# Kernel optimization log

Hardware: AMD Instinct MI355X
Metric: run time of the kernel (lower is better)

Reference implementation:

```python
import jax, jax.numpy as jnp
import numpy as np

POOL = 7  # adaptive_avg_pool2d output size (7,7)


def _bin_edges(start, length):
    """Adaptive-avg-pool bin boundaries.
    start, length: [N] int32 -> (lo, hi) each [N, POOL] absolute indices,
    matching torch: lo_i = floor(i*L/P), hi_i = ceil((i+1)*L/P).
    """
    i = jnp.arange(POOL, dtype=jnp.int32)
    lo = start[:, None] + (i[None, :] * length[:, None]) // POOL
    hi = start[:, None] + (-((-(i[None, :] + 1)) * length[:, None] // POOL))
    # note: ceil(a/b) = -(-a // b); written below explicitly
    hi = start[:, None] - ((-(i[None, :] + 1) * length[:, None]) // POOL)
    return lo, hi


def roi_adaptive_avg_pool(features, rois):
    """features: [1, C, H, W]; rois: [N, 4] int (x1,y1,x2,y2 inclusive).
    Returns [N, C, POOL, POOL] == torch stack of adaptive_avg_pool2d over
    features[:, :, y1:y2+1, x1:x2+1], vectorized via an integral image.
    """
    B, C, H, W = features.shape  # B == 1 (forced by shared_fcs input dim)
    # integral image with a zero row/col prepended: ii[y, x] = sum over [:y, :x]
    ii = jnp.cumsum(jnp.cumsum(features, axis=2), axis=3)
    ii = jnp.pad(ii, ((0, 0), (0, 0), (1, 0), (1, 0)))[0]  # [C, H+1, W+1]

    x1, y1, x2, y2 = rois[:, 0], rois[:, 1], rois[:, 2], rois[:, 3]
    ys, ye = _bin_edges(y1, y2 - y1 + 1)   # [N, POOL]
    xs, xe = _bin_edges(x1, x2 - x1 + 1)
    Y0, Y1 = ys[:, :, None], ye[:, :, None]   # [N, POOL, 1]
    X0, X1 = xs[:, None, :], xe[:, None, :]   # [N, 1, POOL]

    def gather(Y, X):
        return ii[:, Y, X]  # [C, N, POOL, POOL]

    sums = gather(Y1, X1) - gather(Y0, X1) - gather(Y1, X0) + gather(Y0, X0)
    area = ((Y1 - Y0) * (X1 - X0)).astype(features.dtype)  # [N, POOL, POOL]
    pooled = sums / area[None]                              # [C, N, POOL, POOL]
    return jnp.transpose(pooled, (1, 0, 2, 3))              # [N, C, POOL, POOL]


def setup_inputs() -> dict:
    key = jax.random.key(0)
    ks = jax.random.split(key, 12)
    C, H, W, N, F = 256, 336, 336, 2000, 256
    features = jax.random.normal(ks[0], (1, C, H, W), dtype=jnp.float32)
    # valid small ROIs (shuttlecock-sized), x1<=x2, y1<=y2, in-bounds
    x1 = jax.random.randint(ks[1], (N,), 0, W - 40)
    y1 = jax.random.randint(ks[2], (N,), 0, H - 40)
    bw = jax.random.randint(ks[3], (N,), 4, 40)
    bh = jax.random.randint(ks[4], (N,), 4, 40)
    rois = jnp.stack([x1, y1, jnp.minimum(x1 + bw, W - 1),
                      jnp.minimum(y1 + bh, H - 1)], axis=1).astype(jnp.int32)
    d_in = C * POOL * POOL
    w1 = jax.random.normal(ks[5], (d_in, F), dtype=jnp.float32) * (1.0 / np.sqrt(d_in))
    b1 = jnp.zeros((F,), dtype=jnp.float32)
    w2 = jax.random.normal(ks[6], (F, F), dtype=jnp.float32) * (1.0 / np.sqrt(F))
    b2 = jnp.zeros((F,), dtype=jnp.float32)
    w_cls = jax.random.normal(ks[7], (F, 2), dtype=jnp.float32) * 0.01
    b_cls = jnp.zeros((2,), dtype=jnp.float32)
    w_reg = jax.random.normal(ks[8], (F, 4), dtype=jnp.float32) * 0.001
    b_reg = jnp.zeros((4,), dtype=jnp.float32)
    return {"features": features, "rois": rois, "w1": w1, "b1": b1,
            "w2": w2, "b2": b2, "w_cls": w_cls, "b_cls": b_cls,
            "w_reg": w_reg, "b_reg": b_reg}


def reference(features, rois, w1, b1, w2, b2, w_cls, b_cls, w_reg, b_reg):
    roi_feats = roi_adaptive_avg_pool(features, rois)          # [N, C, 7, 7]
    roi_feats = roi_feats.reshape(roi_feats.shape[0], -1)      # [N, C*49]
    h = jax.nn.relu(roi_feats @ w1 + b1)
    h = jax.nn.relu(h @ w2 + b2)
    cls_score = h @ w_cls + b_cls                              # [N, num_classes+1]
    bbox_pred = h @ w_reg + b_reg                              # [N, 4]
    return (cls_score, bbox_pred)
```

## Files before the change

### kernel.cpp

```cpp
#include <hip/hip_runtime.h>

typedef unsigned int uint;
typedef unsigned short ushort;
typedef __bf16 v8bf __attribute__((ext_vector_type(8)));
typedef float v4f __attribute__((ext_vector_type(4)));

#define CCH 256
#define HH 336
#define WW 336
#define HWSZ (HH*WW)
#define NROI 2000
#define KDIM 12544
#define MPAD 2048
#define SPLITK 14
#define KSP (KDIM/SPLITK)

__device__ __forceinline__ ushort bf16r(float f) {
  uint u = __float_as_uint(f);
  u += 0x7fffu + ((u >> 16) & 1u);
  return (ushort)(u >> 16);
}
__device__ __forceinline__ uint packbf(float a, float b) {
  return (uint)bf16r(a) | ((uint)bf16r(b) << 16);
}

typedef const __attribute__((address_space(1))) uint* gas_t;
typedef __attribute__((address_space(3))) uint* las_t;
__device__ __forceinline__ void async16(const void* g, void* l) {
  __builtin_amdgcn_global_load_lds((gas_t)g, (las_t)l, 16, 0, 0);
}

__global__ __launch_bounds__(256) void k_transpose(const float* __restrict__ f,
                                                   uint* __restrict__ ftu) {
  __shared__ uint T[64 * 132];
  int tid = threadIdx.x;
  int hw0 = blockIdx.x * 64;
  int hwl = tid & 63;
  int cq = tid >> 6;
  int hw = hw0 + hwl;
#pragma unroll 4
  for (int it = 0; it < 32; ++it) {
    int c = it * 8 + cq * 2;
    float a = f[(size_t)c * HWSZ + hw];
    float b = f[(size_t)(c + 1) * HWSZ + hw];
    T[hwl * 132 + it * 4 + cq] = packbf(a, b);
  }
  __syncthreads();
  int co = tid & 31, r = tid >> 5;
#pragma unroll
  for (int i = 0; i < 8; ++i) {
    int hwr = i * 8 + r;
    uint4 v = *(const uint4*)&T[hwr * 132 + co * 4];
    *(uint4*)(ftu + (size_t)(hw0 + hwr) * 128 + co * 4) = v;
  }
}

__global__ __launch_bounds__(256) void k_w1perm(const float* __restrict__ w1,
                                                uint* __restrict__ w1t_u) {
  int bin = blockIdx.x % 49;
  int c0 = (blockIdx.x / 49) * 32;
  __shared__ ushort T[32][258];
  int n = threadIdx.x;
  for (int i = 0; i < 32; ++i)
    T[i][n] = bf16r(w1[(size_t)((c0 + i) * 49 + bin) * 256 + n]);
  __syncthreads();
  int cc = threadIdx.x & 15;
  int nb = threadIdx.x >> 4;
  for (int rep = 0; rep < 16; ++rep) {
    int nn = rep * 16 + nb;
    uint v = (uint)T[2 * cc][nn] | ((uint)T[2 * cc + 1][nn] << 16);
    w1t_u[(size_t)nn * (KDIM / 2) + bin * 128 + c0 / 2 + cc] = v;
  }
}

__global__ __launch_bounds__(256) void k_w2t(const float* __restrict__ w2,
                                             ushort* __restrict__ w2t) {
  int n = blockIdx.x, k = threadIdx.x;
  w2t[n * 256 + k] = bf16r(w2[k * 256 + n]);
}

__global__ __launch_bounds__(256) void k_sort(const int* __restrict__ rois,
                                              int* __restrict__ perm) {
  __shared__ int hist[64];
  __shared__ int keys[NROI];
  int tid = threadIdx.x;
  if (tid < 64) hist[tid] = 0;
  __syncthreads();
  for (int i = tid; i < NROI; i += 256) {
    int x1 = rois[i * 4 + 0], y1 = rois[i * 4 + 1];
    int x2 = rois[i * 4 + 2], y2 = rois[i * 4 + 3];
    int cx = (x1 + x2) >> 1, cy = (y1 + y2) >> 1;
    int k = (cy / 42) * 8 + (cx / 42);
    keys[i] = k;
    atomicAdd(&hist[k], 1);
  }
  __syncthreads();
  if (tid == 0) {
    int s = 0;
    for (int b = 0; b < 64; ++b) { int c = hist[b]; hist[b] = s; s += c; }
  }
  __syncthreads();
  for (int i = tid; i < NROI; i += 256) {
    int pos = atomicAdd(&hist[keys[i]], 1);
    perm[pos] = i;
  }
}

#define UNPK8(A, u) do {                                     \
  A[0] += __uint_as_float((u).x << 16);                      \
  A[1] += __uint_as_float((u).x & 0xffff0000u);              \
  A[2] += __uint_as_float((u).y << 16);                      \
  A[3] += __uint_as_float((u).y & 0xffff0000u);              \
  A[4] += __uint_as_float((u).z << 16);                      \
  A[5] += __uint_as_float((u).z & 0xffff0000u);              \
  A[6] += __uint_as_float((u).w << 16);                      \
  A[7] += __uint_as_float((u).w & 0xffff0000u);              \
} while (0)

__global__ __launch_bounds__(64) void k_pool(const int* __restrict__ rois,
                                             const int* __restrict__ perm,
                                             const uint4* __restrict__ ft4,
                                             uint4* __restrict__ rf4) {
  int bx = blockIdx.x;
  int slot = (bx & 7) * 250 + (bx >> 3);
  int n = perm[slot];
  int wv = blockIdx.y;
  int t = threadIdx.x;
  int co = t & 31, par = t >> 5;
  int x1 = rois[n * 4 + 0], y1 = rois[n * 4 + 1];
  int x2 = rois[n * 4 + 2], y2 = rois[n * 4 + 3];
  int Lw = x2 - x1 + 1, Lh = y2 - y1 + 1;
  int ylo = y1 + (wv * Lh) / 7;
  int yhi = y1 + ((wv + 1) * Lh + 6) / 7;
  int rh = yhi - ylo;
  uint ob = (uint)n * 1568 + (uint)wv * 224 + co;
  for (int b = 0; b < 7; ++b) {
    int lo = x1 + (b * Lw) / 7;
    int hi = x1 + ((b + 1) * Lw + 6) / 7;
    float a[8], c[8];
#pragma unroll
    for (int j = 0; j < 8; ++j) { a[j] = 0.f; c[j] = 0.f; }
    for (int y = ylo; y < yhi; ++y) {
      const uint4* p = ft4 + (size_t)(y * WW + lo + par) * 32 + co;
      int x = lo + par;
      for (; x + 2 < hi; x += 4) {
        uint4 u0 = p[0], u1 = p[64];
        p += 128;
        UNPK8(a, u0);
        UNPK8(c, u1);
      }
      for (; x < hi; x += 2) {
        uint4 u = p[0];
        p += 64;
        UNPK8(a, u);
      }
    }
#pragma unroll
    for (int j = 0; j < 8; ++j) a[j] += c[j];
#pragma unroll
    for (int j = 0; j < 8; ++j) a[j] += __shfl_xor(a[j], 32, 64);
    if (t < 32) {
      float inv = 1.0f / (float)(rh * (hi - lo));
      uint4 o;
      o.x = packbf(a[0] * inv, a[1] * inv);
      o.y = packbf(a[2] * inv, a[3] * inv);
      o.z = packbf(a[4] * inv, a[5] * inv);
      o.w = packbf(a[6] * inv, a[7] * inv);
      rf4[ob + b * 32] = o;
    }
  }
}

__global__ __launch_bounds__(256) void k_gemm1(const ushort* __restrict__ A,
                                               const ushort* __restrict__ B,
                                               float* __restrict__ P) {
  __shared__ ushort As[128 * 64];
  __shared__ ushort Bs[128 * 64];
  int m0 = blockIdx.x * 128;
  int n0 = blockIdx.y * 128;
  int ks = blockIdx.z;
  int k0 = ks * KSP;
  int tid = threadIdx.x;
  int lane = tid & 63, wv = tid >> 6;
  int wm = wv >> 1, wn = wv & 1;
  int lm = lane & 15, quad = lane >> 4;
  int srow = tid >> 3, scol = (tid & 7) * 8;
  v4f acc[4][4];
#pragma unroll
  for (int i = 0; i < 4; ++i)
#pragma unroll
    for (int j = 0; j < 4; ++j) acc[i][j] = (v4f){0.f, 0.f, 0.f, 0.f};
  const ushort* Ab = A + (size_t)(m0 + srow) * KDIM + k0 + scol;
  const ushort* Bb = B + (size_t)(n0 + srow) * KDIM + k0 + scol;
  for (int kt = 0; kt < KSP / 64; ++kt) {
    __syncthreads();
#pragma unroll
    for (int r = 0; r < 4; ++r)
      async16(Ab + (size_t)(r * 32) * KDIM + kt * 64, &As[(srow + r * 32) * 64 + scol]);
#pragma unroll
    for (int r = 0; r < 4; ++r)
      async16(Bb + (size_t)(r * 32) * KDIM + kt * 64, &Bs[(srow + r * 32) * 64 + scol]);
    __syncthreads();
#pragma unroll
    for (int kk = 0; kk < 64; kk += 32) {
      v8bf a[4], b[4];
#pragma unroll
      for (int i = 0; i < 4; ++i)
        a[i] = *(const v8bf*)&As[(wm * 64 + i * 16 + lm) * 64 + kk + quad * 8];
#pragma unroll
      for (int j = 0; j < 4; ++j)
        b[j] = *(const v8bf*)&Bs[(wn * 64 + j * 16 + lm) * 64 + kk + quad * 8];
#pragma unroll
      for (int i = 0; i < 4; ++i)
#pragma unroll
        for (int j = 0; j < 4; ++j)
          acc[i][j] = __builtin_amdgcn_mfma_f32_16x16x32_bf16(a[i], b[j], acc[i][j], 0, 0, 0);
    }
  }
  float* Pb = P + (size_t)ks * MPAD * 256;
#pragma unroll
  for (int i = 0; i < 4; ++i)
#pragma unroll
    for (int j = 0; j < 4; ++j) {
      int row = m0 + wm * 64 + i * 16 + quad * 4;
      int col = n0 + wn * 64 + j * 16 + lm;
#pragma unroll
      for (int r = 0; r < 4; ++r)
        Pb[(size_t)(row + r) * 256 + col] = acc[i][j][r];
    }
}

__global__ __launch_bounds__(256) void k_reduce(const float* __restrict__ P,
                                                const float* __restrict__ b1,
                                                uint* __restrict__ h1u) {
  int idx = blockIdx.x * 256 + threadIdx.x;
  int m = idx >> 7, np = idx & 127;
  const float2* Pp = (const float2*)P;
  float2 s = {0.f, 0.f};
#pragma unroll
  for (int ks = 0; ks < SPLITK; ++ks) {
    float2 v = Pp[(size_t)(ks * MPAD + m) * 128 + np];
    s.x += v.x; s.y += v.y;
  }
  s.x += b1[2 * np]; s.y += b1[2 * np + 1];
  s.x = fmaxf(s.x, 0.f); s.y = fmaxf(s.y, 0.f);
  h1u[idx] = packbf(s.x, s.y);
}

__global__ __launch_bounds__(256) void k_gemm2(const ushort* __restrict__ h1b,
                                               const ushort* __restrict__ w2t,
                                               const float* __restrict__ b2,
                                               const float* __restrict__ wcls,
                                               const float* __restrict__ bcls,
                                               const float* __restrict__ wreg,
                                               const float* __restrict__ breg,
                                               float* __restrict__ out) {
  __shared__ ushort As2[64 * 64];
  __shared__ ushort Bs2[256 * 64];
  __shared__ float Hs[64 * 257];
  int tid = threadIdx.x;
  int r0 = blockIdx.x * 64;
  int lane = tid & 63, wv = tid >> 6;
  int lm = lane & 15, quad = lane >> 4;
  int srow = tid >> 3, scol = (tid & 7) * 8;
  v4f acc[16];
#pragma unroll
  for (int j = 0; j < 16; ++j) acc[j] = (v4f){0.f, 0.f, 0.f, 0.f};
  for (int kt = 0; kt < 4; ++kt) {
    __syncthreads();
#pragma unroll
    for (int r = 0; r < 2; ++r)
      async16(h1b + (size_t)(r0 + srow + r * 32) * 256 + kt * 64 + scol,
              &As2[(srow + r * 32) * 64 + scol]);
#pragma unroll
    for (int r = 0; r < 8; ++r)
      async16(w2t + (size_t)(srow + r * 32) * 256 + kt * 64 + scol,
              &Bs2[(srow + r * 32) * 64 + scol]);
    __syncthreads();
#pragma unroll
    for (int kk = 0; kk < 64; kk += 32) {
      v8bf a = *(const v8bf*)&As2[(wv * 16 + lm) * 64 + kk + quad * 8];
#pragma unroll
      for (int j = 0; j < 16; ++j) {
        v8bf b = *(const v8bf*)&Bs2[(j * 16 + lm) * 64 + kk + quad * 8];
        acc[j] = __builtin_amdgcn_mfma_f32_16x16x32_bf16(a, b, acc[j], 0, 0, 0);
      }
    }
  }
#pragma unroll
  for (int j = 0; j < 16; ++j) {
    int nn = j * 16 + lm;
    float bb = b2[nn];
#pragma unroll
    for (int r = 0; r < 4; ++r) {
      int row = wv * 16 + quad * 4 + r;
      Hs[row * 257 + nn] = fmaxf(acc[j][r] + bb, 0.f);
    }
  }
  __syncthreads();
  for (int o = tid; o < 384; o += 256) {
    int hd = o >> 6, r = o & 63;
    int grow = r0 + r;
    float d = 0.f;
    if (hd < 2) {
      for (int k = 0; k < 256; ++k) d += Hs[r * 257 + k] * wcls[k * 2 + hd];
      d += bcls[hd];
      if (grow < NROI) out[grow * 2 + hd] = d;
    } else {
      int h4 = hd - 2;
      for (int k = 0; k < 256; ++k) d += Hs[r * 257 + k] * wreg[k * 4 + h4];
      d += breg[h4];
      if (grow < NROI) out[4000 + grow * 4 + h4] = d;
    }
  }
}

extern "C" void kernel_launch(void* const* d_in, const int* in_sizes, int n_in,
                              void* d_out, int out_size, void* d_ws, size_t ws_size,
                              hipStream_t stream) {
  const float* features = (const float*)d_in[0];
  const int* rois = (const int*)d_in[1];
  const float* w1 = (const float*)d_in[2];
  const float* b1 = (const float*)d_in[3];
  const float* w2 = (const float*)d_in[4];
  const float* b2 = (const float*)d_in[5];
  const float* wcls = (const float*)d_in[6];
  const float* bcls = (const float*)d_in[7];
  const float* wreg = (const float*)d_in[8];
  const float* breg = (const float*)d_in[9];
  char* ws = (char*)d_ws;
  ushort* ft  = (ushort*)(ws + 0);
  ushort* w1t = (ushort*)(ws + 57802752);
  ushort* w2t = (ushort*)(ws + 64225280);
  ushort* rf  = (ushort*)(ws + 64356352);
  int*    perm = (int*)(ws + 64356352 + (size_t)NROI * KDIM * 2);
  float*  P   = (float*)(ws + 115736576);
  ushort* h1b = (ushort*)(ws + 145096704);
  float* out = (float*)d_out;

  hipLaunchKernelGGL(k_transpose, dim3(HWSZ / 64), dim3(256), 0, stream,
                     features, (uint*)ft);
  hipLaunchKernelGGL(k_w1perm, dim3(392), dim3(256), 0, stream, w1, (uint*)w1t);
  hipLaunchKernelGGL(k_w2t, dim3(256), dim3(256), 0, stream, w2, w2t);
  hipLaunchKernelGGL(k_sort, dim3(1), dim3(256), 0, stream, rois, perm);
  hipLaunchKernelGGL(k_pool, dim3(NROI, 7), dim3(64), 0, stream, rois, perm,
                     (const uint4*)ft, (uint4*)rf);
  hipLaunchKernelGGL(k_gemm1, dim3(16, 2, SPLITK), dim3(256), 0, stream, rf, w1t, P);
  hipLaunchKernelGGL(k_reduce, dim3(1024), dim3(256), 0, stream, P, b1, (uint*)h1b);
  hipLaunchKernelGGL(k_gemm2, dim3(32), dim3(256), 0, stream, h1b, w2t, b2, wcls, bcls, wreg, breg, out);
}
```

Baseline: 354.0 us.

## Pad transpose LDS, parallel-scan sort histogram, flatten pool grid, shrink gemm1 M tile

Pads the transpose shared-memory row stride to 134 to cut bank conflicts, reading with two uint2 loads. The histogram prefix sum in the sort kernel becomes a wave-level shuffle scan instead of a serial loop on one thread. The pool kernel uses a 1D grid so the seven row-bins of one ROI get adjacent block indices, which should improve cache locality. gemm1 moves from 128x128 to 64x128 tiles, doubling block count for occupancy at the cost of more B-tile reloads.

```diff
diff --git a/kernel.cpp b/kernel.cpp
--- a/kernel.cpp
+++ b/kernel.cpp
@@ -32,7 +32,7 @@
 
 __global__ __launch_bounds__(256) void k_transpose(const float* __restrict__ f,
                                                    uint* __restrict__ ftu) {
-  __shared__ uint T[64 * 132];
+  __shared__ uint T[64 * 134];
   int tid = threadIdx.x;
   int hw0 = blockIdx.x * 64;
   int hwl = tid & 63;
@@ -43,15 +43,17 @@
     int c = it * 8 + cq * 2;
     float a = f[(size_t)c * HWSZ + hw];
     float b = f[(size_t)(c + 1) * HWSZ + hw];
-    T[hwl * 132 + it * 4 + cq] = packbf(a, b);
+    T[hwl * 134 + it * 4 + cq] = packbf(a, b);
   }
   __syncthreads();
   int co = tid & 31, r = tid >> 5;
 #pragma unroll
   for (int i = 0; i < 8; ++i) {
     int hwr = i * 8 + r;
-    uint4 v = *(const uint4*)&T[hwr * 132 + co * 4];
-    *(uint4*)(ftu + (size_t)(hw0 + hwr) * 128 + co * 4) = v;
+    uint2 v0 = *(const uint2*)&T[hwr * 134 + co * 4];
+    uint2 v1 = *(const uint2*)&T[hwr * 134 + co * 4 + 2];
+    *(uint4*)(ftu + (size_t)(hw0 + hwr) * 128 + co * 4) =
+        make_uint4(v0.x, v0.y, v1.x, v1.y);
   }
 }
 
@@ -95,9 +97,15 @@
     atomicAdd(&hist[k], 1);
   }
   __syncthreads();
-  if (tid == 0) {
-    int s = 0;
-    for (int b = 0; b < 64; ++b) { int c = hist[b]; hist[b] = s; s += c; }
+  if (tid < 64) {
+    int v = hist[tid];
+    int s = v;
+#pragma unroll
+    for (int d = 1; d < 64; d <<= 1) {
+      int t = __shfl_up(s, d, 64);
+      if (tid >= d) s += t;
+    }
+    hist[tid] = s - v;
   }
   __syncthreads();
   for (int i = tid; i < NROI; i += 256) {
@@ -121,19 +129,20 @@
                                              const int* __restrict__ perm,
                                              const uint4* __restrict__ ft4,
                                              uint4* __restrict__ rf4) {
-  int bx = blockIdx.x;
-  int slot = (bx & 7) * 250 + (bx >> 3);
+  int L = blockIdx.x;
+  int i = L >> 3;
+  int slot = (L & 7) * 250 + i / 7;
+  int by = i % 7;
   int n = perm[slot];
-  int wv = blockIdx.y;
   int t = threadIdx.x;
   int co = t & 31, par = t >> 5;
   int x1 = rois[n * 4 + 0], y1 = rois[n * 4 + 1];
   int x2 = rois[n * 4 + 2], y2 = rois[n * 4 + 3];
   int Lw = x2 - x1 + 1, Lh = y2 - y1 + 1;
-  int ylo = y1 + (wv * Lh) / 7;
-  int yhi = y1 + ((wv + 1) * Lh + 6) / 7;
+  int ylo = y1 + (by * Lh) / 7;
+  int yhi = y1 + ((by + 1) * Lh + 6) / 7;
   int rh = yhi - ylo;
-  uint ob = (uint)n * 1568 + (uint)wv * 224 + co;
+  uint ob = (uint)n * 1568 + (uint)by * 224 + co;
   for (int b = 0; b < 7; ++b) {
     int lo = x1 + (b * Lw) / 7;
     int hi = x1 + ((b + 1) * Lw + 6) / 7;
@@ -174,20 +183,20 @@
 __global__ __launch_bounds__(256) void k_gemm1(const ushort* __restrict__ A,
                                                const ushort* __restrict__ B,
                                                float* __restrict__ P) {
-  __shared__ ushort As[128 * 64];
+  __shared__ ushort As[64 * 64];
   __shared__ ushort Bs[128 * 64];
-  int m0 = blockIdx.x * 128;
+  int m0 = blockIdx.x * 64;
   int n0 = blockIdx.y * 128;
   int ks = blockIdx.z;
   int k0 = ks * KSP;
   int tid = threadIdx.x;
   int lane = tid & 63, wv = tid >> 6;
-  int wm = wv >> 1, wn = wv & 1;
+  int wm = wv & 1, wn = wv >> 1;
   int lm = lane & 15, quad = lane >> 4;
   int srow = tid >> 3, scol = (tid & 7) * 8;
-  v4f acc[4][4];
-#pragma unroll
-  for (int i = 0; i < 4; ++i)
+  v4f acc[2][4];
+#pragma unroll
+  for (int i = 0; i < 2; ++i)
 #pragma unroll
     for (int j = 0; j < 4; ++j) acc[i][j] = (v4f){0.f, 0.f, 0.f, 0.f};
   const ushort* Ab = A + (size_t)(m0 + srow) * KDIM + k0 + scol;
@@ -195,7 +204,7 @@
   for (int kt = 0; kt < KSP / 64; ++kt) {
     __syncthreads();
 #pragma unroll
-    for (int r = 0; r < 4; ++r)
+    for (int r = 0; r < 2; ++r)
       async16(Ab + (size_t)(r * 32) * KDIM + kt * 64, &As[(srow + r * 32) * 64 + scol]);
 #pragma unroll
     for (int r = 0; r < 4; ++r)
@@ -203,15 +212,15 @@
     __syncthreads();
 #pragma unroll
     for (int kk = 0; kk < 64; kk += 32) {
-      v8bf a[4], b[4];
-#pragma unroll
-      for (int i = 0; i < 4; ++i)
-        a[i] = *(const v8bf*)&As[(wm * 64 + i * 16 + lm) * 64 + kk + quad * 8];
+      v8bf a[2], b[4];
+#pragma unroll
+      for (int i = 0; i < 2; ++i)
+        a[i] = *(const v8bf*)&As[(wm * 32 + i * 16 + lm) * 64 + kk + quad * 8];
 #pragma unroll
       for (int j = 0; j < 4; ++j)
         b[j] = *(const v8bf*)&Bs[(wn * 64 + j * 16 + lm) * 64 + kk + quad * 8];
 #pragma unroll
-      for (int i = 0; i < 4; ++i)
+      for (int i = 0; i < 2; ++i)
 #pragma unroll
         for (int j = 0; j < 4; ++j)
           acc[i][j] = __builtin_amdgcn_mfma_f32_16x16x32_bf16(a[i], b[j], acc[i][j], 0, 0, 0);
@@ -219,10 +228,10 @@
   }
   float* Pb = P + (size_t)ks * MPAD * 256;
 #pragma unroll
-  for (int i = 0; i < 4; ++i)
+  for (int i = 0; i < 2; ++i)
 #pragma unroll
     for (int j = 0; j < 4; ++j) {
-      int row = m0 + wm * 64 + i * 16 + quad * 4;
+      int row = m0 + wm * 32 + i * 16 + quad * 4;
       int col = n0 + wn * 64 + j * 16 + lm;
 #pragma unroll
       for (int r = 0; r < 4; ++r)
@@ -343,9 +352,9 @@
   hipLaunchKernelGGL(k_w1perm, dim3(392), dim3(256), 0, stream, w1, (uint*)w1t);
   hipLaunchKernelGGL(k_w2t, dim3(256), dim3(256), 0, stream, w2, w2t);
   hipLaunchKernelGGL(k_sort, dim3(1), dim3(256), 0, stream, rois, perm);
-  hipLaunchKernelGGL(k_pool, dim3(NROI, 7), dim3(64), 0, stream, rois, perm,
+  hipLaunchKernelGGL(k_pool, dim3(NROI * 7), dim3(64), 0, stream, rois, perm,
                      (const uint4*)ft, (uint4*)rf);
-  hipLaunchKernelGGL(k_gemm1, dim3(16, 2, SPLITK), dim3(256), 0, stream, rf, w1t, P);
+  hipLaunchKernelGGL(k_gemm1, dim3(32, 2, SPLITK), dim3(256), 0, stream, rf, w1t, P);
   hipLaunchKernelGGL(k_reduce, dim3(1024), dim3(256), 0, stream, P, b1, (uint*)h1b);
   hipLaunchKernelGGL(k_gemm2, dim3(32), dim3(256), 0, stream, h1b, w2t, b2, wcls, bcls, wreg, breg, out);
 }
```

Result: no change. 353.1 us (-0.3%).
